# Performance work log

Hardware: AMD Instinct MI355X
Metric: run time of the kernel (lower is better)

The kernel has to match this reference:

```python
import jax, jax.numpy as jnp
import numpy as np

N = 100_000   # nodes per type
E = 800_000   # edges per relation
H = 128       # hidden_channels
O = 64        # out_channels
TIME_SCALE = 1.0
LN_EPS = 1e-5


def setup_inputs() -> dict:
    key = jax.random.key(0)
    ks = jax.random.split(key, 24)
    nrm = lambda k, shp, s=1.0: jax.random.normal(k, shp, jnp.float32) * s
    inp = {}
    inp["x_A"] = nrm(ks[0], (N, H))
    inp["x_B"] = nrm(ks[1], (N, H))
    inp["x_C"] = nrm(ks[2], (N, H))
    inp["t_A"] = jax.random.uniform(ks[3], (N,), jnp.float32) * 1000.0
    inp["t_B"] = jax.random.uniform(ks[4], (N,), jnp.float32) * 1000.0
    inp["t_C"] = jax.random.uniform(ks[5], (N,), jnp.float32) * 1000.0
    inp["edge1"] = jnp.stack([jax.random.randint(ks[6], (E,), 0, N),
                              jax.random.randint(ks[7], (E,), 0, N)]).astype(jnp.int32)
    inp["edge2"] = jnp.stack([jax.random.randint(ks[8], (E,), 0, N),
                              jax.random.randint(ks[9], (E,), 0, N)]).astype(jnp.int32)
    kk = 10
    for i in range(2):
        inp[f"Wl{i}"] = nrm(ks[kk], (H, H), 0.05); kk += 1
        inp[f"bl{i}"] = jnp.zeros((H,), jnp.float32)
        inp[f"W0{i}"] = nrm(ks[kk], (H, H), 0.05); kk += 1
        inp[f"b0{i}"] = jnp.zeros((H,), jnp.float32)
        inp[f"W1{i}"] = nrm(ks[kk], (H, H), 0.05); kk += 1
        inp[f"b1{i}"] = jnp.zeros((H,), jnp.float32)
        inp[f"gate{i}"] = jnp.asarray(0.5, jnp.float32)
        inp[f"lam{i}"] = jnp.asarray(0.1, jnp.float32)  # raw lambda
        inp[f"lng{i}"] = jnp.ones((H,), jnp.float32)
        inp[f"lnb{i}"] = jnp.zeros((H,), jnp.float32)
    inp["Wout"] = nrm(ks[kk], (H, O), 0.05)
    inp["bout"] = jnp.zeros((O,), jnp.float32)
    return inp


def _layer(h_src, h_dst, x0_dst, edge, t_src, t_dst,
           Wl, bl, W0, b0, W1, b1, gate, raw_lam, lng, lnb):
    s, d = edge[0], edge[1]
    n_dst = h_dst.shape[0]
    # per-edge time-decay weight
    lam = jax.nn.softplus(raw_lam) + 1e-8
    delta = jnp.maximum((t_dst[d] - t_src[s]) / TIME_SCALE, 0.0)
    w = jnp.exp(jnp.maximum(-lam * delta, -60.0))          # [E]
    # gather + weight + scatter-add  (propagate with aggr='add')
    msg = h_src[s] * w[:, None]                            # [E,H]
    agg = jax.ops.segment_sum(msg, d, num_segments=n_dst)  # [n_dst,H]
    deg = jnp.maximum(jax.ops.segment_sum(w, d, num_segments=n_dst), 1e-6)
    out = agg / deg[:, None]
    g = jax.nn.sigmoid(gate)
    y = out @ Wl + bl + (1.0 - g) * (h_dst @ W0 + b0) + g * (x0_dst @ W1 + b1)
    y = jax.nn.relu(y)
    mu = jnp.mean(y, axis=-1, keepdims=True)
    var = jnp.mean((y - mu) ** 2, axis=-1, keepdims=True)
    y = (y - mu) * jax.lax.rsqrt(var + LN_EPS) * lng + lnb
    # index_copy_: only nodes that appear as a destination get updated
    cnt = jax.ops.segment_sum(jnp.ones_like(w), d, num_segments=n_dst)
    return jnp.where((cnt > 0)[:, None], y, h_dst)


def reference(x_A, x_B, x_C, t_A, t_B, t_C, edge1, edge2,
              Wl0, bl0, W00, b00, W10, b10, gate0, lam0, lng0, lnb0,
              Wl1, bl1, W01, b01, W11, b11, gate1, lam1, lng1, lnb1,
              Wout, bout):
    # reversed(metapath): process (B,r2,C) with conv_idx=1 first, then (A,r1,B) with conv_idx=0
    h_C = _layer(x_B, x_C, x_C, edge2, t_B, t_C,
                 Wl1, bl1, W01, b01, W11, b11, gate1, lam1, lng1, lnb1)
    h_B = _layer(x_A, x_B, x_B, edge1, t_A, t_B,
                 Wl0, bl0, W00, b00, W10, b10, gate0, lam0, lng0, lnb0)
    del h_B  # target type is metapath[-1][2] == 'C'; B's update does not feed C
    return h_C @ Wout + bout
```

## Files before the change

kernel.cpp:

```cpp
#include <hip/hip_runtime.h>


#define HD 128
#define OD 64
#define SCAN_E 1024

typedef unsigned short u16;
typedef short v8s __attribute__((ext_vector_type(8)));
typedef float v4f __attribute__((ext_vector_type(4)));

union Frag {
    unsigned int u[4];
    uint4 q;
    v8s v;
};

__device__ __forceinline__ float softplus_f(float x) {
    return fmaxf(x, 0.0f) + log1pf(expf(-fabsf(x)));
}
__device__ __forceinline__ float sigmoid_f(float x) {
    return 1.0f / (1.0f + expf(-x));
}
__device__ __forceinline__ int swz(int r, int c) {
    int g = (c >> 2) ^ (r & 7);
    return r * 128 + g * 4 + (c & 3);
}

__device__ __forceinline__ void gload_lds16(const float* g, float* l) {
    __builtin_amdgcn_global_load_lds(
        (const __attribute__((address_space(1))) void*)g,
        (__attribute__((address_space(3))) void*)l, 16, 0, 0);
}

__device__ __forceinline__ void stage_kc(const float* __restrict__ Asrc, int kc,
                                         float* bufp, int row0, int lane, int N) {
#pragma unroll
    for (int t = 0; t < 4; ++t) {
        int rowL = t * 8 + (lane >> 3);
        int gch  = lane & 7;
        int rG   = row0 + rowL;
        rG = (rG < N) ? rG : (N - 1);
        const float* srcp = Asrc + (size_t)rG * HD + kc * 32 +
                            ((gch ^ (rowL & 7)) << 2);
        gload_lds16(srcp, bufp + t * 256);
    }
}

__device__ __forceinline__ void split_store(float x, u16* ph, u16* pl) {
    unsigned int b = __float_as_uint(x);
    unsigned int h = b & 0xffff0000u;
    *ph = (u16)(h >> 16);
    float r = x - __uint_as_float(h);
    *pl = (u16)(__float_as_uint(r) >> 16);
}

__device__ __forceinline__ void cvt_split8(const float* f, unsigned int* hi,
                                           unsigned int* lo) {
#pragma unroll
    for (int j = 0; j < 4; ++j) {
        unsigned int b0 = __float_as_uint(f[2 * j]);
        unsigned int b1 = __float_as_uint(f[2 * j + 1]);
        unsigned int h0 = b0 & 0xffff0000u;
        unsigned int h1 = b1 & 0xffff0000u;
        hi[j] = (h0 >> 16) | h1;
        float r0 = f[2 * j]     - __uint_as_float(h0);
        float r1 = f[2 * j + 1] - __uint_as_float(h1);
        lo[j] = (__float_as_uint(r0) >> 16) | (__float_as_uint(r1) & 0xffff0000u);
    }
}

__global__ __launch_bounds__(256) void k_prep(
    const int* __restrict__ edge, int* __restrict__ cnt, int E, int gE,
    const float* __restrict__ Wl, const float* __restrict__ W0,
    const float* __restrict__ W1, const float* __restrict__ Wout,
    const float* __restrict__ bl, const float* __restrict__ b0,
    const float* __restrict__ b1, const float* __restrict__ gatep,
    u16* __restrict__ wlh, u16* __restrict__ wll,
    u16* __restrict__ wch, u16* __restrict__ wcl,
    u16* __restrict__ woh, u16* __restrict__ wol, float* __restrict__ bc)
{
    if (blockIdx.x < (unsigned)gE) {
        int e = blockIdx.x * 256 + threadIdx.x;
        if (e < E) atomicAdd(cnt + edge[E + e], 1);
        return;
    }
    int i = (blockIdx.x - gE) * 256 + threadIdx.x;
    const float g = sigmoid_f(gatep[0]);
    if (i < 16384) {
        int n = i >> 7, k = i & 127;
        float a  = Wl[k * 128 + n];
        float w0 = W0[k * 128 + n];
        float w1 = W1[k * 128 + n];
        float c  = (1.f - g) * w0 + g * w1;
        int off = ((k >> 5) * 128 + n) * 32 + (k & 31);
        split_store(a, wlh + off, wll + off);
        split_store(c, wch + off, wcl + off);
    } else if (i < 24576) {
        int j = i - 16384;
        int n = j >> 7, k = j & 127;
        float v = Wout[k * 64 + n];
        int off = ((k >> 5) * 64 + n) * 32 + (k & 31);
        split_store(v, woh + off, wol + off);
    } else if (i < 24704) {
        int t = i - 24576;
        bc[t] = bl[t] + (1.f - g) * b0[t] + g * b1[t];
    }
}

__global__ __launch_bounds__(256) void k_scan1(
    const int* __restrict__ cnt, int* __restrict__ offs,
    int* __restrict__ part, int* __restrict__ tot, int N)
{
    __shared__ int sh[256];
    const int t = threadIdx.x;
    const int base = blockIdx.x * SCAN_E + t * 4;
    int v[4], sum = 0;
#pragma unroll
    for (int i = 0; i < 4; ++i) {
        int idx = base + i;
        v[i] = (idx < N) ? cnt[idx] : 0;
        sum += v[i];
    }
    sh[t] = sum;
    __syncthreads();
    for (int off = 1; off < 256; off <<= 1) {
        int x = (t >= off) ? sh[t - off] : 0;
        __syncthreads();
        sh[t] += x;
        __syncthreads();
    }
    int run = (t > 0) ? sh[t - 1] : 0;
    if (t == 255) part[blockIdx.x] = atomicAdd(tot, sh[255]);
#pragma unroll
    for (int i = 0; i < 4; ++i) {
        int idx = base + i;
        if (idx < N) offs[idx] = run;
        run += v[i];
    }
}

__global__ __launch_bounds__(256) void k_fillw(
    const int* __restrict__ edge, const float* __restrict__ tB,
    const float* __restrict__ tC, const float* __restrict__ lam_raw,
    const int* __restrict__ offs, const int* __restrict__ part,
    int* __restrict__ fillc, int2* __restrict__ srcw, int E)
{
    int e = blockIdx.x * 256 + threadIdx.x;
    if (e >= E) return;
    int s = edge[e];
    int d = edge[E + e];
    float lam = softplus_f(lam_raw[0]) + 1e-8f;
    float dt  = fmaxf(tC[d] - tB[s], 0.0f);
    float w   = expf(fmaxf(-lam * dt, -60.0f));
    int pos = offs[d] + part[d >> 10] + atomicAdd(fillc + d, 1);
    srcw[pos] = make_int2(s, __float_as_int(w));
}

__global__ __launch_bounds__(256) void k_gather(
    const float* __restrict__ xB, const int2* __restrict__ srcw,
    const int* __restrict__ offs, const int* __restrict__ part,
    const int* __restrict__ cnt, float* __restrict__ aggn, int N)
{
    const int wave = (blockIdx.x * 256 + threadIdx.x) >> 6;
    const int lane = threadIdx.x & 63;
    const int slot = lane >> 4;
    const int l4   = lane & 15;
    if (wave >= N) return;
    const int r    = wave;
    const int degc = cnt[r];

    float* dstp = aggn + (size_t)r * HD;
    if (degc == 0) {
        if (slot == 0) {
            *reinterpret_cast<float4*>(dstp + l4 * 4) = make_float4(0, 0, 0, 0);
            *reinterpret_cast<float4*>(dstp + 64 + l4 * 4) = make_float4(0, 0, 0, 0);
        }
        return;
    }

    const int start = offs[r] + part[r >> 10];
    float4 a0 = make_float4(0, 0, 0, 0), a1 = make_float4(0, 0, 0, 0);
    float sw = 0.f;
#pragma unroll 2
    for (int j = slot; j < degc; j += 4) {
        int2 swp = srcw[start + j];
        float w = __int_as_float(swp.y);
        const float* row = xB + (size_t)swp.x * HD;
        float4 x0 = *reinterpret_cast<const float4*>(row + l4 * 4);
        float4 x1 = *reinterpret_cast<const float4*>(row + 64 + l4 * 4);
        a0.x = fmaf(w, x0.x, a0.x); a0.y = fmaf(w, x0.y, a0.y);
        a0.z = fmaf(w, x0.z, a0.z); a0.w = fmaf(w, x0.w, a0.w);
        a1.x = fmaf(w, x1.x, a1.x); a1.y = fmaf(w, x1.y, a1.y);
        a1.z = fmaf(w, x1.z, a1.z); a1.w = fmaf(w, x1.w, a1.w);
        sw += w;
    }
#pragma unroll
    for (int m = 16; m <= 32; m <<= 1) {
        a0.x += __shfl_xor(a0.x, m); a0.y += __shfl_xor(a0.y, m);
        a0.z += __shfl_xor(a0.z, m); a0.w += __shfl_xor(a0.w, m);
        a1.x += __shfl_xor(a1.x, m); a1.y += __shfl_xor(a1.y, m);
        a1.z += __shfl_xor(a1.z, m); a1.w += __shfl_xor(a1.w, m);
        sw   += __shfl_xor(sw, m);
    }
    float inv = 1.0f / fmaxf(sw, 1e-6f);
    if (slot == 0) {
        a0.x *= inv; a0.y *= inv; a0.z *= inv; a0.w *= inv;
        a1.x *= inv; a1.y *= inv; a1.z *= inv; a1.w *= inv;
        *reinterpret_cast<float4*>(dstp + l4 * 4) = a0;
        *reinterpret_cast<float4*>(dstp + 64 + l4 * 4) = a1;
    }
}

__global__ __launch_bounds__(256) void k_fused(
    const float* __restrict__ xC, const float* __restrict__ aggn,
    const int* __restrict__ cnt,
    const u16* __restrict__ wlh, const u16* __restrict__ wll,
    const u16* __restrict__ wch, const u16* __restrict__ wcl,
    const u16* __restrict__ woh, const u16* __restrict__ wol,
    const float* __restrict__ bc, const float* __restrict__ lng,
    const float* __restrict__ lnb, const float* __restrict__ bout,
    float* __restrict__ out, int N)
{
    __shared__ float lds[4 * 2048];

    const int lane = threadIdx.x & 63;
    const int wid  = threadIdx.x >> 6;
    const int lr   = lane & 15;
    const int kb   = lane >> 4;
    const int row0 = blockIdx.x * 128 + wid * 32;
    float* myl = lds + wid * 2048;
    float* st[2] = {myl, myl + 1024};

    v4f acc[2][8] = {};
    const float* As[2] = {aggn, xC};

    stage_kc(As[0], 0, st[0], row0, lane, N);
    int par = 0;
#pragma unroll
    for (int it = 0; it < 8; ++it) {
        const int mat = it >> 2;
        const int kc  = it & 3;
        asm volatile("s_waitcnt vmcnt(0)" ::: "memory");
        if (it < 7) {
            int nit = it + 1;
            stage_kc(As[nit >> 2], nit & 3, st[par ^ 1], row0, lane, N);
        }
        const float* cb = st[par];
        Frag ah[2], al[2];
#pragma unroll
        for (int rt = 0; rt < 2; ++rt) {
            int row = rt * 16 + lr;
            float4 u0 = *reinterpret_cast<const float4*>(
                cb + row * 32 + (((2 * kb)     ^ (row & 7)) << 2));
            float4 u1 = *reinterpret_cast<const float4*>(
                cb + row * 32 + (((2 * kb + 1) ^ (row & 7)) << 2));
            float f[8] = {u0.x, u0.y, u0.z, u0.w, u1.x, u1.y, u1.z, u1.w};
            cvt_split8(f, ah[rt].u, al[rt].u);
        }
        const uint4* BH = (const uint4*)(mat ? wch : wlh);
        const uint4* BL = (const uint4*)(mat ? wcl : wll);
#pragma unroll
        for (int ct = 0; ct < 8; ++ct) {
            int idx = kc * 512 + (ct * 16 + lr) * 4 + kb;
            Frag bh, bl;
            bh.q = BH[idx];
            bl.q = BL[idx];
#pragma unroll
            for (int rt = 0; rt < 2; ++rt) {
                acc[rt][ct] = __builtin_amdgcn_mfma_f32_16x16x32_bf16(
                    ah[rt].v, bh.v, acc[rt][ct], 0, 0, 0);
                acc[rt][ct] = __builtin_amdgcn_mfma_f32_16x16x32_bf16(
                    ah[rt].v, bl.v, acc[rt][ct], 0, 0, 0);
                acc[rt][ct] = __builtin_amdgcn_mfma_f32_16x16x32_bf16(
                    al[rt].v, bh.v, acc[rt][ct], 0, 0, 0);
            }
        }
        par ^= 1;
    }

    float bcv[8], gav[8], bev[8];
#pragma unroll
    for (int ct = 0; ct < 8; ++ct) {
        int c = ct * 16 + lr;
        bcv[ct] = bc[c];
        gav[ct] = lng[c];
        bev[ct] = lnb[c];
    }
    float bov[4];
#pragma unroll
    for (int ct = 0; ct < 4; ++ct) bov[ct] = bout[ct * 16 + lr];

    const uint4* BH3 = (const uint4*)woh;
    const uint4* BL3 = (const uint4*)wol;

#pragma unroll
    for (int rt = 0; rt < 2; ++rt) {
        int rq = row0 + rt * 16 + kb * 4;
        int cvr[4] = {0, 0, 0, 0};
        if (rq < N) {
            int4 cv = *(const int4*)(cnt + rq);
            cvr[0] = cv.x; cvr[1] = cv.y; cvr[2] = cv.z; cvr[3] = cv.w;
        }
#pragma unroll
        for (int reg = 0; reg < 4; ++reg) {
            int rloc = kb * 4 + reg;
            int r    = rq + reg;
            float yv[8];
            float s = 0.f, q = 0.f;
#pragma unroll
            for (int ct = 0; ct < 8; ++ct) {
                float v = acc[rt][ct][reg] + bcv[ct];
                v = fmaxf(v, 0.0f);
                yv[ct] = v;
                s += v;
                q += v * v;
            }
#pragma unroll
            for (int m = 1; m < 16; m <<= 1) {
                s += __shfl_xor(s, m);
                q += __shfl_xor(q, m);
            }
            float mu   = s * (1.0f / 128.0f);
            float var  = q * (1.0f / 128.0f) - mu * mu;
            float rstd = rsqrtf(var + 1e-5f);

            if (r < N) {
                if (cvr[reg] > 0) {
#pragma unroll
                    for (int ct = 0; ct < 8; ++ct)
                        myl[swz(rloc, ct * 16 + lr)] =
                            (yv[ct] - mu) * rstd * gav[ct] + bev[ct];
                } else {
                    size_t base = (size_t)r * HD;
#pragma unroll
                    for (int ct = 0; ct < 8; ++ct)
                        myl[swz(rloc, ct * 16 + lr)] = xC[base + ct * 16 + lr];
                }
            } else {
#pragma unroll
                for (int ct = 0; ct < 8; ++ct)
                    myl[swz(rloc, ct * 16 + lr)] = 0.0f;
            }
        }

        v4f acc2[4] = {};
#pragma unroll
        for (int kc = 0; kc < 4; ++kc) {
            Frag ah, al;
            {
                int c0 = kc * 32 + kb * 8;
                float4 u0 = *reinterpret_cast<const float4*>(&myl[swz(lr, c0)]);
                float4 u1 = *reinterpret_cast<const float4*>(&myl[swz(lr, c0 + 4)]);
                float f[8] = {u0.x, u0.y, u0.z, u0.w, u1.x, u1.y, u1.z, u1.w};
                cvt_split8(f, ah.u, al.u);
            }
#pragma unroll
            for (int ct = 0; ct < 4; ++ct) {
                int idx = kc * 256 + (ct * 16 + lr) * 4 + kb;
                Frag bh, bl;
                bh.q = BH3[idx];
                bl.q = BL3[idx];
                acc2[ct] = __builtin_amdgcn_mfma_f32_16x16x32_bf16(
                    ah.v, bh.v, acc2[ct], 0, 0, 0);
                acc2[ct] = __builtin_amdgcn_mfma_f32_16x16x32_bf16(
                    ah.v, bl.v, acc2[ct], 0, 0, 0);
                acc2[ct] = __builtin_amdgcn_mfma_f32_16x16x32_bf16(
                    al.v, bh.v, acc2[ct], 0, 0, 0);
            }
        }

#pragma unroll
        for (int reg = 0; reg < 4; ++reg) {
            int r = rq + reg;
            if (r < N) {
#pragma unroll
                for (int ct = 0; ct < 4; ++ct)
                    out[(size_t)r * OD + ct * 16 + lr] = acc2[ct][reg] + bov[ct];
            }
        }
    }
}

extern "C" void kernel_launch(void* const* d_in, const int* in_sizes, int n_in,
                              void* d_out, int out_size, void* d_ws, size_t ws_size,
                              hipStream_t stream) {
    const float* xB    = (const float*)d_in[1];
    const float* xC    = (const float*)d_in[2];
    const float* tB    = (const float*)d_in[4];
    const float* tC    = (const float*)d_in[5];
    const int*   edge2 = (const int*)d_in[7];
    const float* Wl1   = (const float*)d_in[18];
    const float* bl1   = (const float*)d_in[19];
    const float* W01   = (const float*)d_in[20];
    const float* b01   = (const float*)d_in[21];
    const float* W11   = (const float*)d_in[22];
    const float* b11   = (const float*)d_in[23];
    const float* gate1 = (const float*)d_in[24];
    const float* lam1  = (const float*)d_in[25];
    const float* lng1  = (const float*)d_in[26];
    const float* lnb1  = (const float*)d_in[27];
    const float* Wout  = (const float*)d_in[28];
    const float* bout  = (const float*)d_in[29];

    const int N = in_sizes[2] / HD;
    const int E = in_sizes[7] / 2;

    int*   cnt   = (int*)d_ws;
    int*   fillc = cnt + N;
    int*   offs  = fillc + N;
    int*   part  = offs + N;
    int*   tot   = part + 128;
    int2*  srcw  = (int2*)(tot + 4);
    u16*   wlh   = (u16*)(srcw + E);
    u16*   wll   = wlh + 16384;
    u16*   wch   = wll + 16384;
    u16*   wcl   = wch + 16384;
    u16*   woh   = wcl + 16384;
    u16*   wol   = woh + 8192;
    float* bc    = (float*)(wol + 8192);
    float* buf   = bc + 128;

    hipMemsetAsync(cnt, 0, (size_t)2 * N * sizeof(int), stream);
    hipMemsetAsync(tot, 0, sizeof(int), stream);

    dim3 blk(256);
    const int gE = (E + 255) / 256;
    const int NB = (N + SCAN_E - 1) / SCAN_E;

    k_prep <<<gE + 97, blk, 0, stream>>>(edge2, cnt, E, gE,
                                         Wl1, W01, W11, Wout, bl1, b01, b11,
                                         gate1, wlh, wll, wch, wcl, woh, wol, bc);
    k_scan1<<<NB, blk, 0, stream>>>(cnt, offs, part, tot, N);
    k_fillw<<<gE, blk, 0, stream>>>(edge2, tB, tC, lam1, offs, part, fillc, srcw, E);

    const int gN64 = (N * 64 + 255) / 256;
    k_gather<<<gN64, blk, 0, stream>>>(xB, srcw, offs, part, cnt, buf, N);

    const int GB = (N + 127) / 128;
    k_fused<<<GB, blk, 0, stream>>>(xC, buf, cnt, wlh, wll, wch, wcl, woh, wol,
                                    bc, lng1, lnb1, bout, (float*)d_out, N);
}
```

Before: 227.5 us.

## Pre-split activations into bf16 hi/lo planes and deepen fused GEMM staging

The gather kernel now writes its normalized aggregate as bf16 hi/lo planes, and k_prep gets extra blocks that pre-split xC the same way. k_fused then loads MFMA-ready fragments straight into LDS with a two-chunk-deep prefetch, so it no longer converts fp32 to split bf16 inside the GEMM loop. The cost is an extra pass over xC plus a separate hi/lo copy of it in memory, while the aggregate buffer stays the same size. The column layout in the gather loads also changes from split halves to contiguous 8-element groups.

```diff
diff --git a/kernel.cpp b/kernel.cpp
--- a/kernel.cpp
+++ b/kernel.cpp
@@ -13,6 +13,7 @@
     unsigned int u[4];
     uint4 q;
     v8s v;
+    u16 h[8];
 };
 
 __device__ __forceinline__ float softplus_f(float x) {
@@ -26,24 +27,10 @@
     return r * 128 + g * 4 + (c & 3);
 }
 
-__device__ __forceinline__ void gload_lds16(const float* g, float* l) {
+__device__ __forceinline__ void gload_lds16(const void* g, void* l) {
     __builtin_amdgcn_global_load_lds(
         (const __attribute__((address_space(1))) void*)g,
         (__attribute__((address_space(3))) void*)l, 16, 0, 0);
-}
-
-__device__ __forceinline__ void stage_kc(const float* __restrict__ Asrc, int kc,
-                                         float* bufp, int row0, int lane, int N) {
-#pragma unroll
-    for (int t = 0; t < 4; ++t) {
-        int rowL = t * 8 + (lane >> 3);
-        int gch  = lane & 7;
-        int rG   = row0 + rowL;
-        rG = (rG < N) ? rG : (N - 1);
-        const float* srcp = Asrc + (size_t)rG * HD + kc * 32 +
-                            ((gch ^ (rowL & 7)) << 2);
-        gload_lds16(srcp, bufp + t * 256);
-    }
 }
 
 __device__ __forceinline__ void split_store(float x, u16* ph, u16* pl) {
@@ -52,6 +39,17 @@
     *ph = (u16)(h >> 16);
     float r = x - __uint_as_float(h);
     *pl = (u16)(__float_as_uint(r) >> 16);
+}
+
+__device__ __forceinline__ void split_pack8(const float* f, Frag* hi, Frag* lo) {
+#pragma unroll
+    for (int j = 0; j < 8; ++j) {
+        unsigned int b = __float_as_uint(f[j]);
+        unsigned int h = b & 0xffff0000u;
+        hi->h[j] = (u16)(h >> 16);
+        float r = f[j] - __uint_as_float(h);
+        lo->h[j] = (u16)(__float_as_uint(r) >> 16);
+    }
 }
 
 __device__ __forceinline__ void cvt_split8(const float* f, unsigned int* hi,
@@ -69,41 +67,72 @@
     }
 }
 
+__device__ __forceinline__ void stage_chunk(
+    const u16* __restrict__ Ah, const u16* __restrict__ Al,
+    int kc, char* buf, int row0w, int lane, int N)
+{
+    const int rfrag = lane & 15;
+    const int kb    = lane >> 4;
+#pragma unroll
+    for (int rt = 0; rt < 2; ++rt) {
+        int rG = row0w + rt * 16 + rfrag;
+        rG = (rG < N) ? rG : (N - 1);
+        size_t so = (size_t)rG * HD + kc * 32 + kb * 8;
+        gload_lds16(Ah + so, buf + rt * 1024);
+        gload_lds16(Al + so, buf + 2048 + rt * 1024);
+    }
+}
+
 __global__ __launch_bounds__(256) void k_prep(
     const int* __restrict__ edge, int* __restrict__ cnt, int E, int gE,
     const float* __restrict__ Wl, const float* __restrict__ W0,
     const float* __restrict__ W1, const float* __restrict__ Wout,
     const float* __restrict__ bl, const float* __restrict__ b0,
     const float* __restrict__ b1, const float* __restrict__ gatep,
+    const float* __restrict__ xC,
     u16* __restrict__ wlh, u16* __restrict__ wll,
     u16* __restrict__ wch, u16* __restrict__ wcl,
-    u16* __restrict__ woh, u16* __restrict__ wol, float* __restrict__ bc)
+    u16* __restrict__ woh, u16* __restrict__ wol, float* __restrict__ bc,
+    u16* __restrict__ xch, u16* __restrict__ xcl, int N)
 {
     if (blockIdx.x < (unsigned)gE) {
         int e = blockIdx.x * 256 + threadIdx.x;
         if (e < E) atomicAdd(cnt + edge[E + e], 1);
         return;
     }
-    int i = (blockIdx.x - gE) * 256 + threadIdx.x;
-    const float g = sigmoid_f(gatep[0]);
-    if (i < 16384) {
-        int n = i >> 7, k = i & 127;
-        float a  = Wl[k * 128 + n];
-        float w0 = W0[k * 128 + n];
-        float w1 = W1[k * 128 + n];
-        float c  = (1.f - g) * w0 + g * w1;
-        int off = ((k >> 5) * 128 + n) * 32 + (k & 31);
-        split_store(a, wlh + off, wll + off);
-        split_store(c, wch + off, wcl + off);
-    } else if (i < 24576) {
-        int j = i - 16384;
-        int n = j >> 7, k = j & 127;
-        float v = Wout[k * 64 + n];
-        int off = ((k >> 5) * 64 + n) * 32 + (k & 31);
-        split_store(v, woh + off, wol + off);
-    } else if (i < 24704) {
-        int t = i - 24576;
-        bc[t] = bl[t] + (1.f - g) * b0[t] + g * b1[t];
+    if (blockIdx.x < (unsigned)(gE + 97)) {
+        int i = (blockIdx.x - gE) * 256 + threadIdx.x;
+        const float g = sigmoid_f(gatep[0]);
+        if (i < 16384) {
+            int n = i >> 7, k = i & 127;
+            float a  = Wl[k * 128 + n];
+            float w0 = W0[k * 128 + n];
+            float w1 = W1[k * 128 + n];
+            float c  = (1.f - g) * w0 + g * w1;
+            int off = ((k >> 5) * 128 + n) * 32 + (k & 31);
+            split_store(a, wlh + off, wll + off);
+            split_store(c, wch + off, wcl + off);
+        } else if (i < 24576) {
+            int j = i - 16384;
+            int n = j >> 7, k = j & 127;
+            float v = Wout[k * 64 + n];
+            int off = ((k >> 5) * 64 + n) * 32 + (k & 31);
+            split_store(v, woh + off, wol + off);
+        } else if (i < 24704) {
+            int t = i - 24576;
+            bc[t] = bl[t] + (1.f - g) * b0[t] + g * b1[t];
+        }
+        return;
+    }
+    long long e8 = ((long long)(blockIdx.x - gE - 97) * 256 + threadIdx.x) * 8;
+    if (e8 < (long long)N * HD) {
+        float4 u0 = *reinterpret_cast<const float4*>(xC + e8);
+        float4 u1 = *reinterpret_cast<const float4*>(xC + e8 + 4);
+        float f[8] = {u0.x, u0.y, u0.z, u0.w, u1.x, u1.y, u1.z, u1.w};
+        Frag hi, lo;
+        split_pack8(f, &hi, &lo);
+        *reinterpret_cast<uint4*>(xch + e8) = hi.q;
+        *reinterpret_cast<uint4*>(xcl + e8) = lo.q;
     }
 }
 
@@ -159,7 +188,8 @@
 __global__ __launch_bounds__(256) void k_gather(
     const float* __restrict__ xB, const int2* __restrict__ srcw,
     const int* __restrict__ offs, const int* __restrict__ part,
-    const int* __restrict__ cnt, float* __restrict__ aggn, int N)
+    const int* __restrict__ cnt, u16* __restrict__ aggh,
+    u16* __restrict__ aggl, int N)
 {
     const int wave = (blockIdx.x * 256 + threadIdx.x) >> 6;
     const int lane = threadIdx.x & 63;
@@ -169,11 +199,11 @@
     const int r    = wave;
     const int degc = cnt[r];
 
-    float* dstp = aggn + (size_t)r * HD;
     if (degc == 0) {
         if (slot == 0) {
-            *reinterpret_cast<float4*>(dstp + l4 * 4) = make_float4(0, 0, 0, 0);
-            *reinterpret_cast<float4*>(dstp + 64 + l4 * 4) = make_float4(0, 0, 0, 0);
+            uint4 z = make_uint4(0, 0, 0, 0);
+            *reinterpret_cast<uint4*>(aggh + (size_t)r * HD + l4 * 8) = z;
+            *reinterpret_cast<uint4*>(aggl + (size_t)r * HD + l4 * 8) = z;
         }
         return;
     }
@@ -185,9 +215,9 @@
     for (int j = slot; j < degc; j += 4) {
         int2 swp = srcw[start + j];
         float w = __int_as_float(swp.y);
-        const float* row = xB + (size_t)swp.x * HD;
-        float4 x0 = *reinterpret_cast<const float4*>(row + l4 * 4);
-        float4 x1 = *reinterpret_cast<const float4*>(row + 64 + l4 * 4);
+        const float* row = xB + (size_t)swp.x * HD + l4 * 8;
+        float4 x0 = *reinterpret_cast<const float4*>(row);
+        float4 x1 = *reinterpret_cast<const float4*>(row + 4);
         a0.x = fmaf(w, x0.x, a0.x); a0.y = fmaf(w, x0.y, a0.y);
         a0.z = fmaf(w, x0.z, a0.z); a0.w = fmaf(w, x0.w, a0.w);
         a1.x = fmaf(w, x1.x, a1.x); a1.y = fmaf(w, x1.y, a1.y);
@@ -204,16 +234,19 @@
     }
     float inv = 1.0f / fmaxf(sw, 1e-6f);
     if (slot == 0) {
-        a0.x *= inv; a0.y *= inv; a0.z *= inv; a0.w *= inv;
-        a1.x *= inv; a1.y *= inv; a1.z *= inv; a1.w *= inv;
-        *reinterpret_cast<float4*>(dstp + l4 * 4) = a0;
-        *reinterpret_cast<float4*>(dstp + 64 + l4 * 4) = a1;
+        float f[8] = {a0.x * inv, a0.y * inv, a0.z * inv, a0.w * inv,
+                      a1.x * inv, a1.y * inv, a1.z * inv, a1.w * inv};
+        Frag hi, lo;
+        split_pack8(f, &hi, &lo);
+        *reinterpret_cast<uint4*>(aggh + (size_t)r * HD + l4 * 8) = hi.q;
+        *reinterpret_cast<uint4*>(aggl + (size_t)r * HD + l4 * 8) = lo.q;
     }
 }
 
 __global__ __launch_bounds__(256) void k_fused(
-    const float* __restrict__ xC, const float* __restrict__ aggn,
-    const int* __restrict__ cnt,
+    const u16* __restrict__ aggh, const u16* __restrict__ aggl,
+    const u16* __restrict__ xch, const u16* __restrict__ xcl,
+    const float* __restrict__ xC, const int* __restrict__ cnt,
     const u16* __restrict__ wlh, const u16* __restrict__ wll,
     const u16* __restrict__ wch, const u16* __restrict__ wcl,
     const u16* __restrict__ woh, const u16* __restrict__ wol,
@@ -221,42 +254,49 @@
     const float* __restrict__ lnb, const float* __restrict__ bout,
     float* __restrict__ out, int N)
 {
-    __shared__ float lds[4 * 2048];
+    __shared__ char lds[32768];
 
     const int lane = threadIdx.x & 63;
     const int wid  = threadIdx.x >> 6;
     const int lr   = lane & 15;
     const int kb   = lane >> 4;
     const int row0 = blockIdx.x * 128 + wid * 32;
-    float* myl = lds + wid * 2048;
-    float* st[2] = {myl, myl + 1024};
+    char* myb = lds + wid * 8192;
+    char* bufs[2] = {myb, myb + 4096};
+
+    const u16* Ahp[2] = {aggh, xch};
+    const u16* Alp[2] = {aggl, xcl};
 
     v4f acc[2][8] = {};
-    const float* As[2] = {aggn, xC};
-
-    stage_kc(As[0], 0, st[0], row0, lane, N);
-    int par = 0;
-#pragma unroll
-    for (int it = 0; it < 8; ++it) {
-        const int mat = it >> 2;
-        const int kc  = it & 3;
-        asm volatile("s_waitcnt vmcnt(0)" ::: "memory");
-        if (it < 7) {
-            int nit = it + 1;
-            stage_kc(As[nit >> 2], nit & 3, st[par ^ 1], row0, lane, N);
-        }
-        const float* cb = st[par];
+
+    stage_chunk(Ahp[0], Alp[0], 0, bufs[0], row0, lane, N);
+    stage_chunk(Ahp[0], Alp[0], 1, bufs[1], row0, lane, N);
+
+#pragma unroll
+    for (int ch = 0; ch < 8; ++ch) {
+        const int mat = ch >> 2, kc = ch & 3;
+        if (ch == 7) {
+            asm volatile("s_waitcnt vmcnt(0)" ::: "memory");
+        } else {
+            asm volatile("s_waitcnt vmcnt(4)" ::: "memory");
+        }
+        const char* cb = bufs[ch & 1];
+
         Frag ah[2], al[2];
 #pragma unroll
         for (int rt = 0; rt < 2; ++rt) {
-            int row = rt * 16 + lr;
-            float4 u0 = *reinterpret_cast<const float4*>(
-                cb + row * 32 + (((2 * kb)     ^ (row & 7)) << 2));
-            float4 u1 = *reinterpret_cast<const float4*>(
-                cb + row * 32 + (((2 * kb + 1) ^ (row & 7)) << 2));
-            float f[8] = {u0.x, u0.y, u0.z, u0.w, u1.x, u1.y, u1.z, u1.w};
-            cvt_split8(f, ah[rt].u, al[rt].u);
-        }
+            ah[rt].q = *reinterpret_cast<const uint4*>(cb + rt * 1024 + lane * 16);
+            al[rt].q = *reinterpret_cast<const uint4*>(cb + 2048 + rt * 1024 + lane * 16);
+        }
+        asm volatile("s_waitcnt lgkmcnt(0)" ::: "memory");
+        __builtin_amdgcn_sched_barrier(0);
+
+        if (ch + 2 < 8) {
+            const int nc = ch + 2;
+            stage_chunk(Ahp[nc >> 2], Alp[nc >> 2], nc & 3,
+                        bufs[ch & 1], row0, lane, N);
+        }
+
         const uint4* BH = (const uint4*)(mat ? wch : wlh);
         const uint4* BL = (const uint4*)(mat ? wcl : wll);
 #pragma unroll
@@ -275,7 +315,6 @@
                     al[rt].v, bh.v, acc[rt][ct], 0, 0, 0);
             }
         }
-        par ^= 1;
     }
 
     float bcv[8], gav[8], bev[8];
@@ -292,6 +331,7 @@
 
     const uint4* BH3 = (const uint4*)woh;
     const uint4* BL3 = (const uint4*)wol;
+    float* hc = (float*)myb;
 
 #pragma unroll
     for (int rt = 0; rt < 2; ++rt) {
@@ -328,18 +368,18 @@
                 if (cvr[reg] > 0) {
 #pragma unroll
                     for (int ct = 0; ct < 8; ++ct)
-                        myl[swz(rloc, ct * 16 + lr)] =
+                        hc[swz(rloc, ct * 16 + lr)] =
                             (yv[ct] - mu) * rstd * gav[ct] + bev[ct];
                 } else {
                     size_t base = (size_t)r * HD;
 #pragma unroll
                     for (int ct = 0; ct < 8; ++ct)
-                        myl[swz(rloc, ct * 16 + lr)] = xC[base + ct * 16 + lr];
+                        hc[swz(rloc, ct * 16 + lr)] = xC[base + ct * 16 + lr];
                 }
             } else {
 #pragma unroll
                 for (int ct = 0; ct < 8; ++ct)
-                    myl[swz(rloc, ct * 16 + lr)] = 0.0f;
+                    hc[swz(rloc, ct * 16 + lr)] = 0.0f;
             }
         }
 
@@ -349,8 +389,8 @@
             Frag ah, al;
             {
                 int c0 = kc * 32 + kb * 8;
-                float4 u0 = *reinterpret_cast<const float4*>(&myl[swz(lr, c0)]);
-                float4 u1 = *reinterpret_cast<const float4*>(&myl[swz(lr, c0 + 4)]);
+                float4 u0 = *reinterpret_cast<const float4*>(&hc[swz(lr, c0)]);
+                float4 u1 = *reinterpret_cast<const float4*>(&hc[swz(lr, c0 + 4)]);
                 float f[8] = {u0.x, u0.y, u0.z, u0.w, u1.x, u1.y, u1.z, u1.w};
                 cvt_split8(f, ah.u, al.u);
             }
@@ -418,7 +458,10 @@
     u16*   woh   = wcl + 16384;
     u16*   wol   = woh + 8192;
     float* bc    = (float*)(wol + 8192);
-    float* buf   = bc + 128;
+    u16*   aggh  = (u16*)(bc + 128);
+    u16*   aggl  = aggh + (size_t)N * HD;
+    u16*   xch   = aggl + (size_t)N * HD;
+    u16*   xcl   = xch + (size_t)N * HD;
 
     hipMemsetAsync(cnt, 0, (size_t)2 * N * sizeof(int), stream);
     hipMemsetAsync(tot, 0, sizeof(int), stream);
@@ -426,17 +469,20 @@
     dim3 blk(256);
     const int gE = (E + 255) / 256;
     const int NB = (N + SCAN_E - 1) / SCAN_E;
-
-    k_prep <<<gE + 97, blk, 0, stream>>>(edge2, cnt, E, gE,
-                                         Wl1, W01, W11, Wout, bl1, b01, b11,
-                                         gate1, wlh, wll, wch, wcl, woh, wol, bc);
+    const int gX = (N * (HD / 8) + 255) / 256;
+
+    k_prep <<<gE + 97 + gX, blk, 0, stream>>>(edge2, cnt, E, gE,
+                                              Wl1, W01, W11, Wout, bl1, b01, b11,
+                                              gate1, xC, wlh, wll, wch, wcl,
+                                              woh, wol, bc, xch, xcl, N);
     k_scan1<<<NB, blk, 0, stream>>>(cnt, offs, part, tot, N);
     k_fillw<<<gE, blk, 0, stream>>>(edge2, tB, tC, lam1, offs, part, fillc, srcw, E);
 
     const int gN64 = (N * 64 + 255) / 256;
-    k_gather<<<gN64, blk, 0, stream>>>(xB, srcw, offs, part, cnt, buf, N);
+    k_gather<<<gN64, blk, 0, stream>>>(xB, srcw, offs, part, cnt, aggh, aggl, N);
 
     const int GB = (N + 127) / 128;
-    k_fused<<<GB, blk, 0, stream>>>(xC, buf, cnt, wlh, wll, wch, wcl, woh, wol,
+    k_fused<<<GB, blk, 0, stream>>>(aggh, aggl, xch, xcl, xC, cnt,
+                                    wlh, wll, wch, wcl, woh, wol,
                                     bc, lng1, lnb1, bout, (float*)d_out, N);
 }
```

Result: slower. 240.0 us (+5.5%).
